# Optimization experiments

Measured on AMD Instinct MI355X. Metric: run time of the kernel, lower is better.

The kernel has to match this reference:

```python
import jax, jax.numpy as jnp
import numpy as np

B, S, E, H = 2, 2048, 1024, 16
D = E // H

def setup_inputs() -> dict:
    key = jax.random.key(0)
    ks = jax.random.split(key, 11)
    sc = 0.02
    inp = {
        'queries': jax.random.normal(ks[0], (B, S, E), jnp.float32),
        'keys':    jax.random.normal(ks[1], (B, S, E), jnp.float32),
        'values':  jax.random.normal(ks[2], (B, S, E), jnp.float32),
        'Wq': jax.random.normal(ks[3], (E, E), jnp.float32) * sc,
        'bq': jnp.zeros((E,), jnp.float32),
        'Wk': jax.random.normal(ks[4], (E, E), jnp.float32) * sc,
        'bk': jnp.zeros((E,), jnp.float32),
        'Wv': jax.random.normal(ks[5], (E, E), jnp.float32) * sc,
        'bv': jnp.zeros((E,), jnp.float32),
        'Wo': jax.random.normal(ks[6], (E, E), jnp.float32) * sc,
        'bo': jnp.zeros((E,), jnp.float32),
        'indicator': 0,
    }
    return inp

def reference(queries, keys, values, Wq, bq, Wk, bk, Wv, bv, Wo, bo, indicator):
    # torch Linear: y = x @ W.T + b
    q = queries @ Wq.T + bq
    k = keys    @ Wk.T + bk
    v = values  @ Wv.T + bv
    # [B,S,E] -> [B,H,S,D]
    q = q.reshape(B, S, H, D).transpose(0, 2, 1, 3)
    k = k.reshape(B, S, H, D).transpose(0, 2, 1, 3)
    v = v.reshape(B, S, H, D).transpose(0, 2, 1, 3)
    scores = jnp.einsum('bhqd,bhkd->bhqk', q, k) / jnp.sqrt(jnp.float32(D))
    w = jax.nn.sigmoid(scores)
    if indicator != 0:
        w = 1.0 - w
    attn = jax.nn.softmax(w, axis=-1)  # dropout_prob=0 -> identity
    out = jnp.einsum('bhqk,bhkd->bhqd', attn, v)
    out = out.transpose(0, 2, 1, 3).reshape(B, S, E)
    return out @ Wo.T + bo
```

## Files before the change

### kernel.cpp

```cpp
#include <hip/hip_runtime.h>
#include <stdint.h>

#define Bb 2
#define Ss 2048
#define Ee 1024
#define Hh 16
#define Dd 64

typedef __bf16 bf16;
typedef __attribute__((ext_vector_type(8))) __bf16 bf16x8;
typedef __attribute__((ext_vector_type(4))) __bf16 bf16x4;
typedef __attribute__((ext_vector_type(4))) float f32x4;

#define MB (1u << 20)
#define OFF_XQ 0u
#define OFF_XK (8u * MB)
#define OFF_XV (16u * MB)
#define OFF_WQ (24u * MB)
#define OFF_WK (26u * MB)
#define OFF_WV (28u * MB)
#define OFF_WO (30u * MB)
#define OFF_Q  (32u * MB)
#define OFF_K  (40u * MB)
#define OFF_VT (48u * MB)
#define OFF_AO (56u * MB)

__device__ __forceinline__ void gll16(const void* g, void* lds) {
  __builtin_amdgcn_global_load_lds(
      (const __attribute__((address_space(1))) void*)g,
      (__attribute__((address_space(3))) void*)lds, 16, 0, 0);
}

__device__ __forceinline__ unsigned pkbf(float lo, float hi) {
  unsigned r;
  asm("v_cvt_pk_bf16_f32 %0, %1, %2" : "=v"(r) : "v"(lo), "v"(hi));
  return r;
}
#define PL32SWAP(a, b) asm("v_permlane32_swap_b32 %0, %1" : "+v"(a), "+v"(b))
#define PL16SWAP(a, b) asm("v_permlane16_swap_b32 %0, %1" : "+v"(a), "+v"(b))

__global__ __launch_bounds__(256) void convert_kernel(
    const float* __restrict__ q, const float* __restrict__ k, const float* __restrict__ v,
    const float* __restrict__ wq, const float* __restrict__ wk, const float* __restrict__ wv,
    const float* __restrict__ wo, char* __restrict__ ws)
{
  const unsigned i = blockIdx.x * 256u + threadIdx.x;
  const float* src;
  bf16* dst;
  float scale = 1.0f;
  if (i < 3145728u) {
    const unsigned a = i >> 20, j = i & 1048575u;
    src = (a == 0 ? q : a == 1 ? k : v) + (size_t)j * 4;
    dst = (bf16*)(ws + (size_t)a * (8u * MB)) + (size_t)j * 4;
  } else {
    const unsigned i2 = i - 3145728u;
    const unsigned a = i2 >> 18, j = i2 & 262143u;
    src = (a == 0 ? wq : a == 1 ? wk : a == 2 ? wv : wo) + (size_t)j * 4;
    dst = (bf16*)(ws + OFF_WQ + (size_t)a * (2u * MB)) + (size_t)j * 4;
    if (a == 0) scale = 0.125f;
  }
  const float4 f = *(const float4*)src;
  bf16x4 o;
  o[0] = (bf16)(f.x * scale);
  o[1] = (bf16)(f.y * scale);
  o[2] = (bf16)(f.z * scale);
  o[3] = (bf16)(f.w * scale);
  *(bf16x4*)dst = o;
}

__device__ __forceinline__ void gemm128_body(
    const bf16* __restrict__ A, const bf16* __restrict__ W,
    char* smem, int m0, int n0, int t, f32x4 (&acc)[4][4])
{
  char* As = smem;
  char* Bs = smem + 16384;
  const int lane = t & 63;
  const int wid = t >> 6;
  const int wm = (wid >> 1) << 6;
  const int wn = (wid & 1) << 6;
  for (int kt = 0; kt < 1024; kt += 64) {
    __syncthreads();
#pragma unroll
    for (int i = 0; i < 4; ++i) {
      const int L = i * 4096 + t * 16;
      const int r = L >> 7;
      const int c = ((L >> 4) & 7) ^ (r & 7);
      gll16(A + (size_t)(m0 + r) * 1024 + kt + c * 8, As + i * 4096 + wid * 1024);
      gll16(W + (size_t)(n0 + r) * 1024 + kt + c * 8, Bs + i * 4096 + wid * 1024);
    }
    __syncthreads();
#pragma unroll
    for (int ks = 0; ks < 2; ++ks) {
      bf16x8 af[4], bff[4];
#pragma unroll
      for (int mi = 0; mi < 4; ++mi) {
        const int r = wm + mi * 16 + (lane & 15);
        const int c = (ks * 4 + (lane >> 4)) ^ (r & 7);
        af[mi] = *(const bf16x8*)(As + r * 128 + c * 16);
      }
#pragma unroll
      for (int ni = 0; ni < 4; ++ni) {
        const int r = wn + ni * 16 + (lane & 15);
        const int c = (ks * 4 + (lane >> 4)) ^ (r & 7);
        bff[ni] = *(const bf16x8*)(Bs + r * 128 + c * 16);
      }
#pragma unroll
      for (int mi = 0; mi < 4; ++mi)
#pragma unroll
        for (int ni = 0; ni < 4; ++ni)
          acc[mi][ni] = __builtin_amdgcn_mfma_f32_16x16x32_bf16(af[mi], bff[ni], acc[mi][ni], 0, 0, 0);
    }
  }
}

__global__ __launch_bounds__(256) void proj_gemm(
    char* __restrict__ ws, const float* __restrict__ bq,
    const float* __restrict__ bk, const float* __restrict__ bv)
{
  __shared__ __align__(16) char smem[32768];
  const int zi = blockIdx.z;
  const bf16* A = (const bf16*)(ws + (zi == 0 ? OFF_XQ : zi == 1 ? OFF_XK : OFF_XV));
  const bf16* W = (const bf16*)(ws + (zi == 0 ? OFF_WQ : zi == 1 ? OFF_WK : OFF_WV));
  const float* bias = zi == 0 ? bq : zi == 1 ? bk : bv;
  bf16* outp = (bf16*)(ws + (zi == 0 ? OFF_Q : zi == 1 ? OFF_K : OFF_VT));
  const float bscale = (zi == 0) ? 0.125f : 1.0f;
  const int t = threadIdx.x;
  const int m0 = blockIdx.y * 128, n0 = blockIdx.x * 128;
  f32x4 acc[4][4] = {};
  gemm128_body(A, W, smem, m0, n0, t, acc);
  const int lane = t & 63, wid = t >> 6;
  const int wm = (wid >> 1) << 6, wn = (wid & 1) << 6;
  const int cl = lane & 15, rl = lane >> 4;
#pragma unroll
  for (int ni = 0; ni < 4; ++ni) {
    const int col = n0 + wn + ni * 16 + cl;
    const float bvv = bias[col] * bscale;
    const int h = col >> 6, d = col & 63;
#pragma unroll
    for (int mi = 0; mi < 4; ++mi) {
      const int row0 = m0 + wm + mi * 16 + rl * 4;
      const int b = row0 >> 11, s = row0 & 2047;
      if (zi == 2) {
        bf16x4 o;
#pragma unroll
        for (int r2 = 0; r2 < 4; ++r2) o[r2] = (bf16)(acc[mi][ni][r2] + bvv);
        *(bf16x4*)&outp[((size_t)((b * Hh + h) * Dd + d) * Ss) + s] = o;
      } else {
#pragma unroll
        for (int r2 = 0; r2 < 4; ++r2) {
          const float val = acc[mi][ni][r2] + bvv;
          outp[((size_t)((b * Hh + h) * Ss + s + r2) * Dd) + d] = (bf16)val;
        }
      }
    }
  }
}

__global__ __launch_bounds__(256, 4) void attn_kernel(char* __restrict__ ws,
                                                      const int* __restrict__ indicator)
{
  __shared__ __align__(16) char smem[40960];
  char* Qs  = smem;
  char* Ks  = smem + 8192;
  char* Vts = smem + 24576;
  char* Os  = smem;
  const int t = threadIdx.x, lane = t & 63, wid = t >> 6;
  const int g = lane >> 4, l15 = lane & 15;
  const int bh = blockIdx.y;
  const int q0 = blockIdx.x * 64;
  const bf16* Qg  = (const bf16*)(ws + OFF_Q)  + (size_t)bh * Ss * Dd;
  const bf16* Kg  = (const bf16*)(ws + OFF_K)  + (size_t)bh * Ss * Dd;
  const bf16* Vtg = (const bf16*)(ws + OFF_VT) + (size_t)bh * Ss * Dd;
  bf16* AO = (bf16*)(ws + OFF_AO);
  const int ind = *indicator;
  const float c1 = (ind != 0) ? 1.44269504f : -1.44269504f;

#pragma unroll
  for (int i = 0; i < 2; ++i) {
    const int L = i * 4096 + t * 16;
    const int r = L >> 7;
    const int c = ((L >> 4) & 7) ^ (r & 7);
    gll16(Qg + (size_t)(q0 + r) * Dd + c * 8, Qs + i * 4096 + wid * 1024);
  }
  __syncthreads();
  bf16x8 qf[2];
#pragma unroll
  for (int ks = 0; ks < 2; ++ks) {
    const int r = wid * 16 + l15;
    const int c = (ks * 4 + g) ^ (r & 7);
    qf[ks] = *(const bf16x8*)(Qs + r * 128 + c * 16);
  }

  f32x4 acc_o[4] = {};
  float psum = 0.0f;

  for (int kt = 0; kt < Ss; kt += 128) {
    __syncthreads();
#pragma unroll
    for (int i = 0; i < 4; ++i) {
      const int L = i * 4096 + t * 16;
      const int r = L >> 7;
      const int c = ((L >> 4) & 7) ^ (r & 7);
      gll16(Kg + (size_t)(kt + r) * Dd + c * 8, Ks + i * 4096 + wid * 1024);
    }
#pragma unroll
    for (int i = 0; i < 4; ++i) {
      const int L = i * 4096 + t * 16;
      const int r = L >> 8;
      const int c = ((L >> 4) & 15) ^ (r & 15);
      gll16(Vtg + (size_t)r * Ss + kt + c * 8, Vts + i * 4096 + wid * 1024);
    }
    __syncthreads();

    f32x4 st[8] = {};
#pragma unroll
    for (int ks = 0; ks < 2; ++ks) {
#pragma unroll
      for (int ni = 0; ni < 8; ++ni) {
        const int r = ni * 16 + l15;
        const int c = (ks * 4 + g) ^ (r & 7);
        const bf16x8 kf = *(const bf16x8*)(Ks + r * 128 + c * 16);
        st[ni] = __builtin_amdgcn_mfma_f32_16x16x32_bf16(kf, qf[ks], st[ni], 0, 0, 0);
      }
    }

#pragma unroll
    for (int kb = 0; kb < 4; ++kb) {
      float p[2][4];
#pragma unroll
      for (int e = 0; e < 2; ++e)
#pragma unroll
        for (int r2 = 0; r2 < 4; ++r2) {
          const float sv = st[2 * kb + e][r2];
          const float ex = __builtin_amdgcn_exp2f(sv * c1);
          const float sig = __builtin_amdgcn_rcpf(1.0f + ex);
          const float pv = __builtin_amdgcn_exp2f(sig * 1.44269504f);
          psum += pv;
          p[e][r2] = pv;
        }
      unsigned E0 = pkbf(p[0][0], p[0][1]);
      unsigned E1 = pkbf(p[0][2], p[0][3]);
      unsigned O0 = pkbf(p[1][0], p[1][1]);
      unsigned O1 = pkbf(p[1][2], p[1][3]);
      PL32SWAP(E0, O0);
      PL16SWAP(E0, O0);
      PL32SWAP(E1, O1);
      PL16SWAP(E1, O1);
      union { unsigned u[4]; bf16x8 v; } pb;
      pb.u[0] = E0; pb.u[1] = E1; pb.u[2] = O0; pb.u[3] = O1;
#pragma unroll
      for (int dblk = 0; dblk < 4; ++dblk) {
        const int r = dblk * 16 + l15;
        const int c = (kb * 4 + g) ^ (r & 15);
        const bf16x8 vf = *(const bf16x8*)(Vts + r * 256 + c * 16);
        acc_o[dblk] = __builtin_amdgcn_mfma_f32_16x16x32_bf16(vf, pb.v, acc_o[dblk], 0, 0, 0);
      }
    }
  }

  psum += __shfl_xor(psum, 16);
  psum += __shfl_xor(psum, 32);
  const float rinv = __builtin_amdgcn_rcpf(psum);

  __syncthreads();
  {
    const int row = wid * 16 + l15;
#pragma unroll
    for (int dblk = 0; dblk < 4; ++dblk) {
      const unsigned w0 = pkbf(acc_o[dblk][0] * rinv, acc_o[dblk][1] * rinv);
      const unsigned w1 = pkbf(acc_o[dblk][2] * rinv, acc_o[dblk][3] * rinv);
      const int cc = dblk * 2 + (g >> 1);
      char* a = Os + row * 128 + (cc ^ (row & 7)) * 16 + (g & 1) * 8;
      *(uint2*)a = make_uint2(w0, w1);
    }
  }
  __syncthreads();
  const int b = bh >> 4, h = bh & 15;
#pragma unroll
  for (int i = 0; i < 2; ++i) {
    const int L = i * 4096 + t * 16;
    const int r = L >> 7;
    const int cc = (L >> 4) & 7;
    const uint2 w = *(const uint2*)(Os + r * 128 + (cc ^ (r & 7)) * 16);
    const uint2 w2 = *(const uint2*)(Os + r * 128 + (cc ^ (r & 7)) * 16 + 8);
    bf16* dst = &AO[((size_t)(b * Ss + q0 + r) << 10) + h * 64 + cc * 8];
    *(uint2*)dst = w;
    *(uint2*)(dst + 4) = w2;
  }
}

__global__ __launch_bounds__(256) void out_gemm(char* __restrict__ ws,
                                                const float* __restrict__ bo,
                                                float* __restrict__ outp)
{
  __shared__ __align__(16) char smem[32768];
  const bf16* A = (const bf16*)(ws + OFF_AO);
  const bf16* W = (const bf16*)(ws + OFF_WO);
  const int t = threadIdx.x;
  const int m0 = blockIdx.y * 128, n0 = blockIdx.x * 128;
  f32x4 acc[4][4] = {};
  gemm128_body(A, W, smem, m0, n0, t, acc);
  const int lane = t & 63, wid = t >> 6;
  const int wm = (wid >> 1) << 6, wn = (wid & 1) << 6;
  const int cl = lane & 15, rl = lane >> 4;
#pragma unroll
  for (int ni = 0; ni < 4; ++ni) {
    const int col = n0 + wn + ni * 16 + cl;
    const float bvv = bo[col];
#pragma unroll
    for (int mi = 0; mi < 4; ++mi)
#pragma unroll
      for (int r2 = 0; r2 < 4; ++r2) {
        const int row = m0 + wm + mi * 16 + rl * 4 + r2;
        outp[(size_t)row * Ee + col] = acc[mi][ni][r2] + bvv;
      }
  }
}

extern "C" void kernel_launch(void* const* d_in, const int* in_sizes, int n_in,
                              void* d_out, int out_size, void* d_ws, size_t ws_size,
                              hipStream_t stream) {
  (void)in_sizes; (void)n_in; (void)out_size; (void)ws_size;
  const float* queries = (const float*)d_in[0];
  const float* keys    = (const float*)d_in[1];
  const float* values  = (const float*)d_in[2];
  const float* Wq = (const float*)d_in[3];
  const float* bq = (const float*)d_in[4];
  const float* Wk = (const float*)d_in[5];
  const float* bk = (const float*)d_in[6];
  const float* Wv = (const float*)d_in[7];
  const float* bv = (const float*)d_in[8];
  const float* Wo = (const float*)d_in[9];
  const float* bo = (const float*)d_in[10];
  const int* indicator = (const int*)d_in[11];
  char* ws = (char*)d_ws;
  float* outp = (float*)d_out;

  convert_kernel<<<16384, 256, 0, stream>>>(queries, keys, values, Wq, Wk, Wv, Wo, ws);
  proj_gemm<<<dim3(8, 32, 3), 256, 0, stream>>>(ws, bq, bk, bv);
  attn_kernel<<<dim3(32, 32), 256, 0, stream>>>(ws, indicator);
  out_gemm<<<dim3(8, 32), 256, 0, stream>>>(ws, bo, outp);
}
```

Baseline: 253.9 us.

## Fold sigmoid constants into Q, double attention query tile, MFMA row sums, narrower out GEMM

The ±log2(e) factor for the sigmoid is folded into the Q weight and bias scaling, so the attention kernel drops its per-score multiply. The exp(sigmoid) is rewritten as exp2 of a reciprocal with a constant offset, and the score accumulators start at a folded bias constant. Each attention block now handles 128 query rows (two 16-row halves per wave), so every K/V tile loaded into LDS is reused twice, at the cost of more registers and occupancy lowered to 2. Row sums move from shuffle reductions to an MFMA against a ones vector. s_setprio hints are added around the MFMA loops, and the output GEMM switches to 128x64 tiles to launch more blocks.

```diff
diff --git a/kernel.cpp b/kernel.cpp
--- a/kernel.cpp
+++ b/kernel.cpp
@@ -42,7 +42,7 @@
 __global__ __launch_bounds__(256) void convert_kernel(
     const float* __restrict__ q, const float* __restrict__ k, const float* __restrict__ v,
     const float* __restrict__ wq, const float* __restrict__ wk, const float* __restrict__ wv,
-    const float* __restrict__ wo, char* __restrict__ ws)
+    const float* __restrict__ wo, const int* __restrict__ ind, char* __restrict__ ws)
 {
   const unsigned i = blockIdx.x * 256u + threadIdx.x;
   const float* src;
@@ -57,7 +57,10 @@
     const unsigned a = i2 >> 18, j = i2 & 262143u;
     src = (a == 0 ? wq : a == 1 ? wk : a == 2 ? wv : wo) + (size_t)j * 4;
     dst = (bf16*)(ws + OFF_WQ + (size_t)a * (2u * MB)) + (size_t)j * 4;
-    if (a == 0) scale = 0.125f;
+    if (a == 0) {
+      const float c1v = (*ind != 0) ? 1.442695041f : -1.442695041f;
+      scale = 0.125f * c1v;
+    }
   }
   const float4 f = *(const float4*)src;
   bf16x4 o;
@@ -104,18 +107,21 @@
         const int c = (ks * 4 + (lane >> 4)) ^ (r & 7);
         bff[ni] = *(const bf16x8*)(Bs + r * 128 + c * 16);
       }
+      __builtin_amdgcn_s_setprio(1);
 #pragma unroll
       for (int mi = 0; mi < 4; ++mi)
 #pragma unroll
         for (int ni = 0; ni < 4; ++ni)
           acc[mi][ni] = __builtin_amdgcn_mfma_f32_16x16x32_bf16(af[mi], bff[ni], acc[mi][ni], 0, 0, 0);
+      __builtin_amdgcn_s_setprio(0);
     }
   }
 }
 
 __global__ __launch_bounds__(256) void proj_gemm(
     char* __restrict__ ws, const float* __restrict__ bq,
-    const float* __restrict__ bk, const float* __restrict__ bv)
+    const float* __restrict__ bk, const float* __restrict__ bv,
+    const int* __restrict__ ind)
 {
   __shared__ __align__(16) char smem[32768];
   const int zi = blockIdx.z;
@@ -123,7 +129,8 @@
   const bf16* W = (const bf16*)(ws + (zi == 0 ? OFF_WQ : zi == 1 ? OFF_WK : OFF_WV));
   const float* bias = zi == 0 ? bq : zi == 1 ? bk : bv;
   bf16* outp = (bf16*)(ws + (zi == 0 ? OFF_Q : zi == 1 ? OFF_K : OFF_VT));
-  const float bscale = (zi == 0) ? 0.125f : 1.0f;
+  const float c1v = (*ind != 0) ? 1.442695041f : -1.442695041f;
+  const float bscale = (zi == 0) ? 0.125f * c1v : 1.0f;
   const int t = threadIdx.x;
   const int m0 = blockIdx.y * 128, n0 = blockIdx.x * 128;
   f32x4 acc[4][4] = {};
@@ -156,43 +163,45 @@
   }
 }
 
-__global__ __launch_bounds__(256, 4) void attn_kernel(char* __restrict__ ws,
-                                                      const int* __restrict__ indicator)
+__global__ __launch_bounds__(256, 2) void attn_kernel(char* __restrict__ ws)
 {
-  __shared__ __align__(16) char smem[40960];
+  __shared__ __align__(16) char smem[49152];
   char* Qs  = smem;
-  char* Ks  = smem + 8192;
-  char* Vts = smem + 24576;
+  char* Ks  = smem + 16384;
+  char* Vts = smem + 32768;
   char* Os  = smem;
   const int t = threadIdx.x, lane = t & 63, wid = t >> 6;
   const int g = lane >> 4, l15 = lane & 15;
   const int bh = blockIdx.y;
-  const int q0 = blockIdx.x * 64;
+  const int q0 = blockIdx.x * 128;
   const bf16* Qg  = (const bf16*)(ws + OFF_Q)  + (size_t)bh * Ss * Dd;
   const bf16* Kg  = (const bf16*)(ws + OFF_K)  + (size_t)bh * Ss * Dd;
   const bf16* Vtg = (const bf16*)(ws + OFF_VT) + (size_t)bh * Ss * Dd;
   bf16* AO = (bf16*)(ws + OFF_AO);
-  const int ind = *indicator;
-  const float c1 = (ind != 0) ? 1.44269504f : -1.44269504f;
-
-#pragma unroll
-  for (int i = 0; i < 2; ++i) {
+
+#pragma unroll
+  for (int i = 0; i < 4; ++i) {
     const int L = i * 4096 + t * 16;
     const int r = L >> 7;
     const int c = ((L >> 4) & 7) ^ (r & 7);
     gll16(Qg + (size_t)(q0 + r) * Dd + c * 8, Qs + i * 4096 + wid * 1024);
   }
   __syncthreads();
-  bf16x8 qf[2];
-#pragma unroll
-  for (int ks = 0; ks < 2; ++ks) {
-    const int r = wid * 16 + l15;
-    const int c = (ks * 4 + g) ^ (r & 7);
-    qf[ks] = *(const bf16x8*)(Qs + r * 128 + c * 16);
-  }
-
-  f32x4 acc_o[4] = {};
-  float psum = 0.0f;
+  bf16x8 qf[2][2];
+#pragma unroll
+  for (int qh = 0; qh < 2; ++qh)
+#pragma unroll
+    for (int ks = 0; ks < 2; ++ks) {
+      const int r = wid * 32 + qh * 16 + l15;
+      const int c = (ks * 4 + g) ^ (r & 7);
+      qf[qh][ks] = *(const bf16x8*)(Qs + r * 128 + c * 16);
+    }
+
+  f32x4 acc_o[2][4] = {};
+  f32x4 acc_sum[2] = {};
+  union { unsigned u[4]; bf16x8 v; } ones_;
+#pragma unroll
+  for (int j = 0; j < 4; ++j) ones_.u[j] = 0x3F803F80u;
 
   for (int kt = 0; kt < Ss; kt += 128) {
     __syncthreads();
@@ -212,7 +221,13 @@
     }
     __syncthreads();
 
-    f32x4 st[8] = {};
+    f32x4 st[2][8];
+#pragma unroll
+    for (int qh = 0; qh < 2; ++qh)
+#pragma unroll
+      for (int ni = 0; ni < 8; ++ni)
+        st[qh][ni] = (f32x4){-0.52876637f, -0.52876637f, -0.52876637f, -0.52876637f};
+    __builtin_amdgcn_s_setprio(1);
 #pragma unroll
     for (int ks = 0; ks < 2; ++ks) {
 #pragma unroll
@@ -220,55 +235,62 @@
         const int r = ni * 16 + l15;
         const int c = (ks * 4 + g) ^ (r & 7);
         const bf16x8 kf = *(const bf16x8*)(Ks + r * 128 + c * 16);
-        st[ni] = __builtin_amdgcn_mfma_f32_16x16x32_bf16(kf, qf[ks], st[ni], 0, 0, 0);
-      }
-    }
+        st[0][ni] = __builtin_amdgcn_mfma_f32_16x16x32_bf16(kf, qf[0][ks], st[0][ni], 0, 0, 0);
+        st[1][ni] = __builtin_amdgcn_mfma_f32_16x16x32_bf16(kf, qf[1][ks], st[1][ni], 0, 0, 0);
+      }
+    }
+    __builtin_amdgcn_s_setprio(0);
 
 #pragma unroll
     for (int kb = 0; kb < 4; ++kb) {
-      float p[2][4];
-#pragma unroll
-      for (int e = 0; e < 2; ++e)
-#pragma unroll
-        for (int r2 = 0; r2 < 4; ++r2) {
-          const float sv = st[2 * kb + e][r2];
-          const float ex = __builtin_amdgcn_exp2f(sv * c1);
-          const float sig = __builtin_amdgcn_rcpf(1.0f + ex);
-          const float pv = __builtin_amdgcn_exp2f(sig * 1.44269504f);
-          psum += pv;
-          p[e][r2] = pv;
-        }
-      unsigned E0 = pkbf(p[0][0], p[0][1]);
-      unsigned E1 = pkbf(p[0][2], p[0][3]);
-      unsigned O0 = pkbf(p[1][0], p[1][1]);
-      unsigned O1 = pkbf(p[1][2], p[1][3]);
-      PL32SWAP(E0, O0);
-      PL16SWAP(E0, O0);
-      PL32SWAP(E1, O1);
-      PL16SWAP(E1, O1);
-      union { unsigned u[4]; bf16x8 v; } pb;
-      pb.u[0] = E0; pb.u[1] = E1; pb.u[2] = O0; pb.u[3] = O1;
+      union { unsigned u[4]; bf16x8 v; } pb[2];
+#pragma unroll
+      for (int qh = 0; qh < 2; ++qh) {
+        float p[2][4];
+#pragma unroll
+        for (int e = 0; e < 2; ++e)
+#pragma unroll
+          for (int r2 = 0; r2 < 4; ++r2) {
+            const float ex = __builtin_amdgcn_exp2f(st[qh][2 * kb + e][r2]);
+            const float tt = __builtin_amdgcn_rcpf(0.69314718f + ex);
+            p[e][r2] = __builtin_amdgcn_exp2f(tt);
+          }
+        unsigned E0 = pkbf(p[0][0], p[0][1]);
+        unsigned E1 = pkbf(p[0][2], p[0][3]);
+        unsigned O0 = pkbf(p[1][0], p[1][1]);
+        unsigned O1 = pkbf(p[1][2], p[1][3]);
+        PL32SWAP(E0, O0);
+        PL16SWAP(E0, O0);
+        PL32SWAP(E1, O1);
+        PL16SWAP(E1, O1);
+        pb[qh].u[0] = E0; pb[qh].u[1] = E1; pb[qh].u[2] = O0; pb[qh].u[3] = O1;
+      }
+      __builtin_amdgcn_s_setprio(1);
 #pragma unroll
       for (int dblk = 0; dblk < 4; ++dblk) {
         const int r = dblk * 16 + l15;
         const int c = (kb * 4 + g) ^ (r & 15);
         const bf16x8 vf = *(const bf16x8*)(Vts + r * 256 + c * 16);
-        acc_o[dblk] = __builtin_amdgcn_mfma_f32_16x16x32_bf16(vf, pb.v, acc_o[dblk], 0, 0, 0);
-      }
-    }
-  }
-
-  psum += __shfl_xor(psum, 16);
-  psum += __shfl_xor(psum, 32);
-  const float rinv = __builtin_amdgcn_rcpf(psum);
+        acc_o[0][dblk] = __builtin_amdgcn_mfma_f32_16x16x32_bf16(vf, pb[0].v, acc_o[0][dblk], 0, 0, 0);
+        acc_o[1][dblk] = __builtin_amdgcn_mfma_f32_16x16x32_bf16(vf, pb[1].v, acc_o[1][dblk], 0, 0, 0);
+      }
+      acc_sum[0] = __builtin_amdgcn_mfma_f32_16x16x32_bf16(ones_.v, pb[0].v, acc_sum[0], 0, 0, 0);
+      acc_sum[1] = __builtin_amdgcn_mfma_f32_16x16x32_bf16(ones_.v, pb[1].v, acc_sum[1], 0, 0, 0);
+      __builtin_amdgcn_s_setprio(0);
+    }
+  }
+
+  const float rinv[2] = {__builtin_amdgcn_rcpf(acc_sum[0][0]),
+                         __builtin_amdgcn_rcpf(acc_sum[1][0])};
 
   __syncthreads();
-  {
-    const int row = wid * 16 + l15;
+#pragma unroll
+  for (int qh = 0; qh < 2; ++qh) {
+    const int row = wid * 32 + qh * 16 + l15;
 #pragma unroll
     for (int dblk = 0; dblk < 4; ++dblk) {
-      const unsigned w0 = pkbf(acc_o[dblk][0] * rinv, acc_o[dblk][1] * rinv);
-      const unsigned w1 = pkbf(acc_o[dblk][2] * rinv, acc_o[dblk][3] * rinv);
+      const unsigned w0 = pkbf(acc_o[qh][dblk][0] * rinv[qh], acc_o[qh][dblk][1] * rinv[qh]);
+      const unsigned w1 = pkbf(acc_o[qh][dblk][2] * rinv[qh], acc_o[qh][dblk][3] * rinv[qh]);
       const int cc = dblk * 2 + (g >> 1);
       char* a = Os + row * 128 + (cc ^ (row & 7)) * 16 + (g & 1) * 8;
       *(uint2*)a = make_uint2(w0, w1);
@@ -277,15 +299,12 @@
   __syncthreads();
   const int b = bh >> 4, h = bh & 15;
 #pragma unroll
-  for (int i = 0; i < 2; ++i) {
+  for (int i = 0; i < 4; ++i) {
     const int L = i * 4096 + t * 16;
     const int r = L >> 7;
     const int cc = (L >> 4) & 7;
-    const uint2 w = *(const uint2*)(Os + r * 128 + (cc ^ (r & 7)) * 16);
-    const uint2 w2 = *(const uint2*)(Os + r * 128 + (cc ^ (r & 7)) * 16 + 8);
-    bf16* dst = &AO[((size_t)(b * Ss + q0 + r) << 10) + h * 64 + cc * 8];
-    *(uint2*)dst = w;
-    *(uint2*)(dst + 4) = w2;
+    const uint4 w = *(const uint4*)(Os + r * 128 + (cc ^ (r & 7)) * 16);
+    *(uint4*)&AO[((size_t)(b * Ss + q0 + r) << 10) + h * 64 + cc * 8] = w;
   }
 }
 
@@ -293,25 +312,67 @@
                                                 const float* __restrict__ bo,
                                                 float* __restrict__ outp)
 {
-  __shared__ __align__(16) char smem[32768];
+  __shared__ __align__(16) char smem[24576];
+  char* As = smem;
+  char* Bs = smem + 16384;
   const bf16* A = (const bf16*)(ws + OFF_AO);
   const bf16* W = (const bf16*)(ws + OFF_WO);
-  const int t = threadIdx.x;
-  const int m0 = blockIdx.y * 128, n0 = blockIdx.x * 128;
-  f32x4 acc[4][4] = {};
-  gemm128_body(A, W, smem, m0, n0, t, acc);
-  const int lane = t & 63, wid = t >> 6;
-  const int wm = (wid >> 1) << 6, wn = (wid & 1) << 6;
-  const int cl = lane & 15, rl = lane >> 4;
-#pragma unroll
-  for (int ni = 0; ni < 4; ++ni) {
-    const int col = n0 + wn + ni * 16 + cl;
+  const int t = threadIdx.x, lane = t & 63, wid = t >> 6;
+  const int l15 = lane & 15, g = lane >> 4;
+  const int m0 = blockIdx.y * 128, n0 = blockIdx.x * 64;
+  const int wm = (wid >> 1) << 6;
+  const int wn = (wid & 1) << 5;
+  f32x4 acc[4][2] = {};
+  for (int kt = 0; kt < 1024; kt += 64) {
+    __syncthreads();
+#pragma unroll
+    for (int i = 0; i < 4; ++i) {
+      const int L = i * 4096 + t * 16;
+      const int r = L >> 7;
+      const int c = ((L >> 4) & 7) ^ (r & 7);
+      gll16(A + (size_t)(m0 + r) * 1024 + kt + c * 8, As + i * 4096 + wid * 1024);
+    }
+#pragma unroll
+    for (int i = 0; i < 2; ++i) {
+      const int L = i * 4096 + t * 16;
+      const int r = L >> 7;
+      const int c = ((L >> 4) & 7) ^ (r & 7);
+      gll16(W + (size_t)(n0 + r) * 1024 + kt + c * 8, Bs + i * 4096 + wid * 1024);
+    }
+    __syncthreads();
+#pragma unroll
+    for (int ks = 0; ks < 2; ++ks) {
+      bf16x8 af[4], bff[2];
+#pragma unroll
+      for (int mi = 0; mi < 4; ++mi) {
+        const int r = wm + mi * 16 + l15;
+        const int c = (ks * 4 + g) ^ (r & 7);
+        af[mi] = *(const bf16x8*)(As + r * 128 + c * 16);
+      }
+#pragma unroll
+      for (int ni = 0; ni < 2; ++ni) {
+        const int r = wn + ni * 16 + l15;
+        const int c = (ks * 4 + g) ^ (r & 7);
+        bff[ni] = *(const bf16x8*)(Bs + r * 128 + c * 16);
+      }
+      __builtin_amdgcn_s_setprio(1);
+#pragma unroll
+      for (int mi = 0; mi < 4; ++mi)
+#pragma unroll
+        for (int ni = 0; ni < 2; ++ni)
+          acc[mi][ni] = __builtin_amdgcn_mfma_f32_16x16x32_bf16(af[mi], bff[ni], acc[mi][ni], 0, 0, 0);
+      __builtin_amdgcn_s_setprio(0);
+    }
+  }
+#pragma unroll
+  for (int ni = 0; ni < 2; ++ni) {
+    const int col = n0 + wn + ni * 16 + l15;
     const float bvv = bo[col];
 #pragma unroll
     for (int mi = 0; mi < 4; ++mi)
 #pragma unroll
       for (int r2 = 0; r2 < 4; ++r2) {
-        const int row = m0 + wm + mi * 16 + rl * 4 + r2;
+        const int row = m0 + wm + mi * 16 + g * 4 + r2;
         outp[(size_t)row * Ee + col] = acc[mi][ni][r2] + bvv;
       }
   }
@@ -336,8 +397,8 @@
   char* ws = (char*)d_ws;
   float* outp = (float*)d_out;
 
-  convert_kernel<<<16384, 256, 0, stream>>>(queries, keys, values, Wq, Wk, Wv, Wo, ws);
-  proj_gemm<<<dim3(8, 32, 3), 256, 0, stream>>>(ws, bq, bk, bv);
-  attn_kernel<<<dim3(32, 32), 256, 0, stream>>>(ws, indicator);
-  out_gemm<<<dim3(8, 32), 256, 0, stream>>>(ws, bo, outp);
-}
+  convert_kernel<<<16384, 256, 0, stream>>>(queries, keys, values, Wq, Wk, Wv, Wo, indicator, ws);
+  proj_gemm<<<dim3(8, 32, 3), 256, 0, stream>>>(ws, bq, bk, bv, indicator);
+  attn_kernel<<<dim3(16, 32), 256, 0, stream>>>(ws);
+  out_gemm<<<dim3(16, 32), 256, 0, stream>>>(ws, bo, outp);
+}
```

Measured after the change: 235.9 us. 1.08x faster.
